# Kernel optimization log

Hardware: AMD Instinct MI355X
Metric: run time of the kernel (lower is better)

Reference implementation:

```python
import jax, jax.numpy as jnp
import numpy as np

DIM = 768
NUM_PROMPTS = 10
LATENT = 20
B = 16
N = 4096
EPS = 1e-5


def quick_gelu(x):
    return x * jax.nn.sigmoid(1.702 * x)


def layer_norm(x, g, b):
    mu = jnp.mean(x, axis=-1, keepdims=True)
    var = jnp.var(x, axis=-1, keepdims=True)
    return (x - mu) * jax.lax.rsqrt(var + EPS) * g + b


def setup_inputs() -> dict:
    key = jax.random.key(0)
    ks = jax.random.split(key, 12)
    s_in = 1.0 / np.sqrt(DIM)
    s_lat = 1.0 / np.sqrt(LATENT)
    s64 = 1.0 / np.sqrt(64)
    return {
        "x": jax.random.normal(ks[0], (B, NUM_PROMPTS + 1 + N, DIM), jnp.float32),
        "local_tokens": jax.random.normal(ks[1], (B, N, DIM), jnp.float32),
        # proj_down: Linear(dim, latent)
        "Wd": jax.random.uniform(ks[2], (DIM, LATENT), jnp.float32, -s_in, s_in),
        "bd": jnp.zeros((LATENT,), jnp.float32),
        # proj_up: Linear(latent, dim)
        "Wu": jax.random.uniform(ks[3], (LATENT, DIM), jnp.float32, -s_lat, s_lat),
        "bu": jnp.zeros((DIM,), jnp.float32),
        # global / local query projections: Linear(latent, latent)
        "Wgq": jax.random.uniform(ks[4], (LATENT, LATENT), jnp.float32, -s_lat, s_lat),
        "bgq": jnp.zeros((LATENT,), jnp.float32),
        "Wlq": jax.random.uniform(ks[5], (LATENT, LATENT), jnp.float32, -s_lat, s_lat),
        "blq": jnp.zeros((LATENT,), jnp.float32),
        # cls_analyzer: LN(latent) -> Linear(latent,64) -> GELU -> Linear(64,num_prompts) -> Sigmoid
        "ln_c_g": jnp.ones((LATENT,), jnp.float32),
        "ln_c_b": jnp.zeros((LATENT,), jnp.float32),
        "Wc1": jax.random.uniform(ks[6], (LATENT, 64), jnp.float32, -s_lat, s_lat),
        "bc1": jnp.zeros((64,), jnp.float32),
        "Wc2": jax.random.uniform(ks[7], (64, NUM_PROMPTS), jnp.float32, -s64, s64),
        "bc2": jnp.zeros((NUM_PROMPTS,), jnp.float32),
        # gl_balancer: LN(latent) -> Linear(latent,1) -> Sigmoid
        "ln_g_g": jnp.ones((LATENT,), jnp.float32),
        "ln_g_b": jnp.zeros((LATENT,), jnp.float32),
        "Wg": jax.random.uniform(ks[8], (LATENT, 1), jnp.float32, -s_lat, s_lat),
        "bg": jnp.zeros((1,), jnp.float32),
    }


def _attend(q, tokens, scale):
    # q: [B,P,d], tokens: [B,n,d]
    w = jax.nn.softmax(jnp.einsum('bpd,bnd->bpn', q, tokens) * scale, axis=-1)
    return jnp.einsum('bpn,bnd->bpd', w, tokens)


def reference(x, local_tokens, Wd, bd, Wu, bu, Wgq, bgq, Wlq, blq,
              ln_c_g, ln_c_b, Wc1, bc1, Wc2, bc2, ln_g_g, ln_g_b, Wg, bg):
    scale = LATENT ** (-0.5)
    x_latent = quick_gelu(x @ Wd + bd)            # [B, P+1+N, d]
    local_latent = quick_gelu(local_tokens @ Wd + bd)  # [B, N, d]

    prompts_latent = x_latent[:, :NUM_PROMPTS]              # [B,P,d]
    cls_latent = x_latent[:, NUM_PROMPTS:NUM_PROMPTS + 1]   # [B,1,d]
    global_img_latent = x_latent[:, NUM_PROMPTS + 1:]       # [B,N,d]

    cls_ln = layer_norm(cls_latent, ln_c_g, ln_c_b)
    prompt_importance = jax.nn.sigmoid(
        jax.nn.gelu(cls_ln @ Wc1 + bc1, approximate=False) @ Wc2 + bc2)  # [B,1,P]
    global_weight = jax.nn.sigmoid(layer_norm(cls_latent, ln_g_g, ln_g_b) @ Wg + bg)  # [B,1,1]

    global_context = _attend(prompts_latent @ Wgq + bgq, global_img_latent, scale)
    local_context = _attend(prompts_latent @ Wlq + blq, local_latent, scale)

    fused = global_weight * global_context + (1.0 - global_weight) * local_context
    enhanced = fused * jnp.swapaxes(prompt_importance, 1, 2)  # [B,P,d]

    combined = jnp.concatenate([enhanced, cls_latent, global_img_latent], axis=1)
    return combined @ Wu + bu
```

## Files before the change

### kernel.cpp

```cpp
#include <hip/hip_runtime.h>
#include <math.h>

#define DIM   768
#define LAT   20
#define NP    10
#define NB    16
#define SEQ   4096
#define SEQX  (NP + 1 + SEQ)
#define NXROWS (NB * SEQX)
#define NLROWS (NB * SEQ)
#define NROWS  (NXROWS + NLROWS)
#define EPSF  1e-5f

typedef __attribute__((ext_vector_type(8))) short  v8s;
typedef __attribute__((ext_vector_type(4))) float  v4f;
typedef __attribute__((ext_vector_type(4))) unsigned short u16x4;
typedef __attribute__((ext_vector_type(8))) unsigned short u16x8;

__device__ __forceinline__ float sigmoidf_(float z) { return 1.f / (1.f + __expf(-z)); }

__device__ __forceinline__ unsigned short bf16u(float v) {
    unsigned u = __builtin_bit_cast(unsigned, v);
    unsigned r = u + 0x7fffu + ((u >> 16) & 1u);
    return (unsigned short)(r >> 16);
}

__device__ __forceinline__ void gload_lds16(const void* g, void* s) {
    __builtin_amdgcn_global_load_lds(
        (const __attribute__((address_space(1))) unsigned int*)g,
        (__attribute__((address_space(3))) unsigned int*)s, 16, 0, 0);
}

__global__ __launch_bounds__(256) void k_wfrag(const float* __restrict__ Wd,
                                               unsigned short* __restrict__ wf)
{
    int slot = blockIdx.x * 256 + threadIdx.x;
    int fs = slot >> 7, rem = slot & 127;
    int nt = rem >> 6, l = rem & 63;
    int n = nt * 16 + (l & 15);
    int q = l >> 4;
    u16x8 w;
#pragma unroll
    for (int e = 0; e < 8; e++) {
        int k = fs * 32 + q * 8 + e;
        float v = (n < LAT) ? Wd[k * LAT + n] : 0.f;
        w[e] = bf16u(v);
    }
    *(u16x8*)&wf[slot * 8] = w;
}

#define WF_B    49152
#define SLOT_B  2048
#define RING_B  (4 * SLOT_B)

__global__ __launch_bounds__(256, 2) void k_down(const float* __restrict__ x,
                                                 const float* __restrict__ loc,
                                                 const unsigned short* __restrict__ wf,
                                                 const float* __restrict__ bd,
                                                 float* __restrict__ lat)
{
    __shared__ __align__(16) unsigned short lds[(WF_B + 4 * RING_B) / 2];
    const int tid = threadIdx.x, l = tid & 63, w = tid >> 6;

    {
        const char* g = (const char*)wf;
        char* s = (char*)lds;
#pragma unroll
        for (int i = 0; i < 12; ++i) {
            int off = i * 4096 + w * 1024;
            gload_lds16(g + off + l * 16, s + off);
        }
    }
    asm volatile("s_waitcnt vmcnt(0)" ::: "memory");
    __syncthreads();

    const int r0 = blockIdx.x * 64 + w * 16;
    if (r0 >= NROWS) return;
    const float* srcb = (r0 < NXROWS) ? x + (size_t)r0 * DIM
                                      : loc + (size_t)(r0 - NXROWS) * DIM;
    const float* gp = srcb + (size_t)(l & 15) * DIM + (l >> 4) * 8;
    char* ring = (char*)lds + WF_B + w * RING_B;

#pragma unroll
    for (int p = 0; p < 4; ++p) {
        gload_lds16(gp + p * 32,     ring + p * SLOT_B);
        gload_lds16(gp + p * 32 + 4, ring + p * SLOT_B + 1024);
    }

    v4f acc0 = {0.f, 0.f, 0.f, 0.f}, acc1 = {0.f, 0.f, 0.f, 0.f};

#define CVT8(A, F0, F1)                                                   \
    A[0] = (short)bf16u(F0.x); A[1] = (short)bf16u(F0.y);                 \
    A[2] = (short)bf16u(F0.z); A[3] = (short)bf16u(F0.w);                 \
    A[4] = (short)bf16u(F1.x); A[5] = (short)bf16u(F1.y);                 \
    A[6] = (short)bf16u(F1.z); A[7] = (short)bf16u(F1.w);

#define KSTEP(T, VMSTR) do {                                              \
    asm volatile("s_waitcnt " VMSTR ::: "memory");                        \
    float4 f0 = *(const float4*)(ring + ((T) & 3) * SLOT_B + l * 16);     \
    float4 f1 = *(const float4*)(ring + ((T) & 3) * SLOT_B + 1024 + l * 16); \
    v8s a; CVT8(a, f0, f1);                                               \
    v8s b0 = *(const v8s*)&lds[(((T) * 2 + 0) * 64 + l) * 8];             \
    v8s b1 = *(const v8s*)&lds[(((T) * 2 + 1) * 64 + l) * 8];             \
    acc0 = __builtin_amdgcn_mfma_f32_16x16x32_bf16(a, b0, acc0, 0, 0, 0); \
    acc1 = __builtin_amdgcn_mfma_f32_16x16x32_bf16(a, b1, acc1, 0, 0, 0); \
    if ((T) + 4 < 24) {                                                   \
        asm volatile("s_waitcnt lgkmcnt(0)" ::: "memory");                \
        gload_lds16(gp + ((T) + 4) * 32,     ring + ((T) & 3) * SLOT_B);  \
        gload_lds16(gp + ((T) + 4) * 32 + 4, ring + ((T) & 3) * SLOT_B + 1024); \
    }                                                                     \
} while (0)

    KSTEP(0,  "vmcnt(6)");  KSTEP(1,  "vmcnt(6)");  KSTEP(2,  "vmcnt(6)");
    KSTEP(3,  "vmcnt(6)");  KSTEP(4,  "vmcnt(6)");  KSTEP(5,  "vmcnt(6)");
    KSTEP(6,  "vmcnt(6)");  KSTEP(7,  "vmcnt(6)");  KSTEP(8,  "vmcnt(6)");
    KSTEP(9,  "vmcnt(6)");  KSTEP(10, "vmcnt(6)");  KSTEP(11, "vmcnt(6)");
    KSTEP(12, "vmcnt(6)");  KSTEP(13, "vmcnt(6)");  KSTEP(14, "vmcnt(6)");
    KSTEP(15, "vmcnt(6)");  KSTEP(16, "vmcnt(6)");  KSTEP(17, "vmcnt(6)");
    KSTEP(18, "vmcnt(6)");  KSTEP(19, "vmcnt(6)");  KSTEP(20, "vmcnt(6)");
    KSTEP(21, "vmcnt(4)");  KSTEP(22, "vmcnt(2)");  KSTEP(23, "vmcnt(0)");
#undef KSTEP
#undef CVT8

    int col = l & 15, half = l >> 4;
#pragma unroll
    for (int nt = 0; nt < 2; nt++) {
        int j = nt * 16 + col;
        if (j >= LAT) continue;
        float bdj = bd[j];
        v4f A = nt ? acc1 : acc0;
#pragma unroll
        for (int r = 0; r < 4; r++) {
            int rowg = r0 + half * 4 + r;
            float z = A[r] + bdj;
            lat[(size_t)rowg * LAT + j] = z * sigmoidf_(1.702f * z);
        }
    }
}

__global__ __launch_bounds__(192, 3) void k_up(const float* __restrict__ lat,
                                               const float* __restrict__ Wu,
                                               const float* __restrict__ bu,
                                               float* __restrict__ out)
{
    int t = threadIdx.x;
    float4 wu[LAT];
#pragma unroll
    for (int k = 0; k < LAT; k++) wu[k] = ((const float4*)Wu)[k * 192 + t];
    float4 bv = ((const float4*)bu)[t];

    __shared__ float latile[64 * LAT];
    int rowbase = blockIdx.x * 64;
    {
        const float4* src = (const float4*)(lat + (size_t)rowbase * LAT);
        for (int idx = t; idx < 320; idx += 192) ((float4*)latile)[idx] = src[idx];
    }
    __syncthreads();

    int idx0 = rowbase % SEQX;
    for (int i = 0; i < 64; i++) {
        int row = rowbase + i;
        if (row >= NXROWS) break;
        int idx = idx0 + i;
        if (idx >= SEQX) idx -= SEQX;
        if (idx < NP) continue;
        const float* lp = latile + i * LAT;
        float4 acc = bv;
#pragma unroll
        for (int k = 0; k < LAT; k++) {
            float v = lp[k];
            acc.x += v * wu[k].x; acc.y += v * wu[k].y;
            acc.z += v * wu[k].z; acc.w += v * wu[k].w;
        }
        ((float4*)out)[(size_t)row * 192 + t] = acc;
    }
}

__global__ __launch_bounds__(64) void k_small(const float* __restrict__ lat_x,
    const float* __restrict__ Wgq, const float* __restrict__ bgq,
    const float* __restrict__ Wlq, const float* __restrict__ blq,
    const float* __restrict__ lncg, const float* __restrict__ lncb,
    const float* __restrict__ Wc1, const float* __restrict__ bc1,
    const float* __restrict__ Wc2, const float* __restrict__ bc2,
    const float* __restrict__ lngg, const float* __restrict__ lngb,
    const float* __restrict__ Wg, const float* __restrict__ bg,
    float* __restrict__ qg, float* __restrict__ ql,
    float* __restrict__ imp, float* __restrict__ gw)
{
    int b = blockIdx.x, t = threadIdx.x;
    __shared__ float cls[LAT], clsln[LAT], h1[64];
    __shared__ float mu_s, rs_s;

    const float* cp = lat_x + (size_t)(b * SEQX + NP) * LAT;
    if (t < LAT) cls[t] = cp[t];
    __syncthreads();

    if (t == 0) {
        float m = 0.f;
        for (int k = 0; k < LAT; k++) m += cls[k];
        m /= LAT;
        float v = 0.f;
        for (int k = 0; k < LAT; k++) { float d = cls[k] - m; v += d * d; }
        v /= LAT;
        float rs = rsqrtf(v + EPSF);
        mu_s = m; rs_s = rs;
        float s = bg[0];
        for (int k = 0; k < LAT; k++)
            s += ((cls[k] - m) * rs * lngg[k] + lngb[k]) * Wg[k];
        gw[b] = sigmoidf_(s);
    }
    __syncthreads();
    if (t < LAT) clsln[t] = (cls[t] - mu_s) * rs_s * lncg[t] + lncb[t];
    __syncthreads();

    {
        float s = bc1[t];
        for (int k = 0; k < LAT; k++) s += clsln[k] * Wc1[k * 64 + t];
        h1[t] = 0.5f * s * (1.f + erff(s * 0.70710678118f));
    }
    __syncthreads();
    if (t < NP) {
        float s = bc2[t];
        for (int i = 0; i < 64; i++) s += h1[i] * Wc2[i * NP + t];
        imp[b * NP + t] = sigmoidf_(s);
    }
    for (int idx = t; idx < NP * LAT; idx += 64) {
        int p = idx / LAT, j = idx % LAT;
        const float* pl = lat_x + (size_t)(b * SEQX + p) * LAT;
        float sg = bgq[j], sl = blq[j];
        for (int k = 0; k < LAT; k++) {
            float v = pl[k];
            sg += v * Wgq[k * LAT + j];
            sl += v * Wlq[k * LAT + j];
        }
        qg[(b * NP + p) * LAT + j] = sg;
        ql[(b * NP + p) * LAT + j] = sl;
    }
}

__global__ __launch_bounds__(256) void k_attn(const float* __restrict__ lat_x,
                                              const float* __restrict__ lat_l,
                                              const float* __restrict__ qg,
                                              const float* __restrict__ ql,
                                              float* __restrict__ ctxg,
                                              float* __restrict__ ctxl)
{
    int b = blockIdx.x, p = blockIdx.y, ty = blockIdx.z;
    const float* tok = (ty == 0) ? lat_x + (size_t)(b * SEQX + NP + 1) * LAT
                                 : lat_l + (size_t)b * SEQ * LAT;
    const float* q = ((ty == 0) ? qg : ql) + (size_t)(b * NP + p) * LAT;
    float* ctx = ((ty == 0) ? ctxg : ctxl) + (size_t)(b * NP + p) * LAT;

    int t = threadIdx.x;
    __shared__ float qs[LAT];
    __shared__ float red[128];
    __shared__ float Ms;
    __shared__ float tot[21];
    if (t < LAT) qs[t] = q[t];
    __syncthreads();

    const float scale = 0.22360679775f;
    float lg[16];
    float lmax = -1e30f;
    for (int i = 0; i < 16; i++) {
        const float* tk = tok + (size_t)(t + 256 * i) * LAT;
        float s = 0.f;
#pragma unroll
        for (int k = 0; k < LAT; k++) s += qs[k] * tk[k];
        s *= scale;
        lg[i] = s;
        lmax = fmaxf(lmax, s);
    }
    int wave = t >> 6, lane = t & 63;
    for (int off = 32; off; off >>= 1) lmax = fmaxf(lmax, __shfl_down(lmax, off, 64));
    if (lane == 0) red[wave] = lmax;
    __syncthreads();
    if (t == 0) Ms = fmaxf(fmaxf(red[0], red[1]), fmaxf(red[2], red[3]));
    __syncthreads();
    float M = Ms;

    float vals[21];
#pragma unroll
    for (int j = 0; j < 21; j++) vals[j] = 0.f;
    for (int i = 0; i < 16; i++) {
        float w = __expf(lg[i] - M);
        vals[20] += w;
        const float* tk = tok + (size_t)(t + 256 * i) * LAT;
#pragma unroll
        for (int k = 0; k < LAT; k++) vals[k] += w * tk[k];
    }
#pragma unroll
    for (int j = 0; j < 21; j++) {
        float v = vals[j];
        for (int off = 32; off; off >>= 1) v += __shfl_down(v, off, 64);
        vals[j] = v;
    }
    __syncthreads();
    if (lane == 0)
        for (int j = 0; j < 21; j++) red[wave * 21 + j] = vals[j];
    __syncthreads();
    if (t < 21) tot[t] = red[t] + red[21 + t] + red[42 + t] + red[63 + t];
    __syncthreads();
    if (t < LAT) ctx[t] = tot[t] / tot[20];
}

__global__ __launch_bounds__(192) void k_prompt_out(const float* __restrict__ ctxg,
                                                    const float* __restrict__ ctxl,
                                                    const float* __restrict__ imp,
                                                    const float* __restrict__ gw,
                                                    const float* __restrict__ Wu,
                                                    const float* __restrict__ bu,
                                                    float* __restrict__ out)
{
    int b = blockIdx.x, p = blockIdx.y, t = threadIdx.x;
    __shared__ float enh[LAT];
    if (t < LAT) {
        float g = gw[b];
        size_t o = (size_t)(b * NP + p) * LAT + t;
        float e = g * ctxg[o] + (1.f - g) * ctxl[o];
        enh[t] = e * imp[b * NP + p];
    }
    __syncthreads();
    float4 acc = ((const float4*)bu)[t];
#pragma unroll
    for (int k = 0; k < LAT; k++) {
        float4 w = ((const float4*)Wu)[k * 192 + t];
        float e = enh[k];
        acc.x += e * w.x; acc.y += e * w.y; acc.z += e * w.z; acc.w += e * w.w;
    }
    ((float4*)out)[(size_t)(b * SEQX + p) * 192 + t] = acc;
}

extern "C" void kernel_launch(void* const* d_in, const int* in_sizes, int n_in,
                              void* d_out, int out_size, void* d_ws, size_t ws_size,
                              hipStream_t stream)
{
    const float* x    = (const float*)d_in[0];
    const float* loc  = (const float*)d_in[1];
    const float* Wd   = (const float*)d_in[2];
    const float* bd   = (const float*)d_in[3];
    const float* Wu   = (const float*)d_in[4];
    const float* bu   = (const float*)d_in[5];
    const float* Wgq  = (const float*)d_in[6];
    const float* bgq  = (const float*)d_in[7];
    const float* Wlq  = (const float*)d_in[8];
    const float* blq  = (const float*)d_in[9];
    const float* lncg = (const float*)d_in[10];
    const float* lncb = (const float*)d_in[11];
    const float* Wc1  = (const float*)d_in[12];
    const float* bc1  = (const float*)d_in[13];
    const float* Wc2  = (const float*)d_in[14];
    const float* bc2  = (const float*)d_in[15];
    const float* lngg = (const float*)d_in[16];
    const float* lngb = (const float*)d_in[17];
    const float* Wg   = (const float*)d_in[18];
    const float* bg   = (const float*)d_in[19];
    float* out = (float*)d_out;

    float* ws   = (float*)d_ws;
    float* lat_x = ws;
    float* lat_l = lat_x + (size_t)NXROWS * LAT;
    float* qg    = lat_l + (size_t)NLROWS * LAT;
    float* ql    = qg + NB * NP * LAT;
    float* ctxg  = ql + NB * NP * LAT;
    float* ctxl  = ctxg + NB * NP * LAT;
    float* impw  = ctxl + NB * NP * LAT;
    float* gww   = impw + NB * NP;
    unsigned short* wfrag = (unsigned short*)(gww + NB);

    k_wfrag<<<12, 256, 0, stream>>>(Wd, wfrag);
    k_down<<<(NROWS + 63) / 64, 256, 0, stream>>>(x, loc, wfrag, bd, lat_x);
    k_up<<<(NXROWS + 63) / 64, 192, 0, stream>>>(lat_x, Wu, bu, out);
    k_small<<<NB, 64, 0, stream>>>(lat_x, Wgq, bgq, Wlq, blq, lncg, lncb,
                                   Wc1, bc1, Wc2, bc2, lngg, lngb, Wg, bg,
                                   qg, ql, impw, gww);
    k_attn<<<dim3(NB, NP, 2), 256, 0, stream>>>(lat_x, lat_l, qg, ql, ctxg, ctxl);
    k_prompt_out<<<dim3(NB, NP), 192, 0, stream>>>(ctxg, ctxl, impw, gww, Wu, bu, out);
}
```

Measured before the change: 566.3 us.

## Restructure k_down staging into swizzled row-contiguous chunks with packed bf16 convert

The down-projection kernel now stages each 16-row block of input in 64-float chunks. Each lane loads contiguous 16-byte pieces of a row into an XOR-swizzled LDS layout with a two-slot double buffer, which replaces the previous scattered per-lane 16-byte loads. The float-to-bf16 conversion uses the hardware packed instruction v_cvt_pk_bf16_f32 instead of manual integer rounding. The up-projection kernel reads each latent row with five vector LDS loads instead of scalar reads. The aim is better global-load coalescing and fewer ALU instructions, at the cost of more complex addressing and a shallower prefetch depth in waits.

```diff
diff --git a/kernel.cpp b/kernel.cpp
--- a/kernel.cpp
+++ b/kernel.cpp
@@ -14,7 +14,7 @@
 
 typedef __attribute__((ext_vector_type(8))) short  v8s;
 typedef __attribute__((ext_vector_type(4))) float  v4f;
-typedef __attribute__((ext_vector_type(4))) unsigned short u16x4;
+typedef __attribute__((ext_vector_type(4))) unsigned int u32x4;
 typedef __attribute__((ext_vector_type(8))) unsigned short u16x8;
 
 __device__ __forceinline__ float sigmoidf_(float z) { return 1.f / (1.f + __expf(-z)); }
@@ -23,6 +23,12 @@
     unsigned u = __builtin_bit_cast(unsigned, v);
     unsigned r = u + 0x7fffu + ((u >> 16) & 1u);
     return (unsigned short)(r >> 16);
+}
+
+__device__ __forceinline__ unsigned cvtpk(float lo, float hi) {
+    unsigned r;
+    asm("v_cvt_pk_bf16_f32 %0, %1, %2" : "=v"(r) : "v"(lo), "v"(hi));
+    return r;
 }
 
 __device__ __forceinline__ void gload_lds16(const void* g, void* s) {
@@ -50,8 +56,7 @@
 }
 
 #define WF_B    49152
-#define SLOT_B  2048
-#define RING_B  (4 * SLOT_B)
+#define RING0   WF_B
 
 __global__ __launch_bounds__(256, 2) void k_down(const float* __restrict__ x,
                                                  const float* __restrict__ loc,
@@ -59,7 +64,7 @@
                                                  const float* __restrict__ bd,
                                                  float* __restrict__ lat)
 {
-    __shared__ __align__(16) unsigned short lds[(WF_B + 4 * RING_B) / 2];
+    __shared__ __align__(16) unsigned short lds[(WF_B + 4 * 8192) / 2];
     const int tid = threadIdx.x, l = tid & 63, w = tid >> 6;
 
     {
@@ -78,49 +83,70 @@
     if (r0 >= NROWS) return;
     const float* srcb = (r0 < NXROWS) ? x + (size_t)r0 * DIM
                                       : loc + (size_t)(r0 - NXROWS) * DIM;
-    const float* gp = srcb + (size_t)(l & 15) * DIM + (l >> 4) * 8;
-    char* ring = (char*)lds + WF_B + w * RING_B;
-
-#pragma unroll
-    for (int p = 0; p < 4; ++p) {
-        gload_lds16(gp + p * 32,     ring + p * SLOT_B);
-        gload_lds16(gp + p * 32 + 4, ring + p * SLOT_B + 1024);
-    }
+
+    const int rrq = l >> 4, cc = l & 15;
+    const float* Pp[4];
+#pragma unroll
+    for (int i = 0; i < 4; ++i) {
+        int rr = i * 4 + rrq;
+        Pp[i] = srcb + (size_t)rr * DIM + ((cc ^ (rr & 7)) * 4);
+    }
+
+    unsigned Aadr[2][2][2];
+    {
+        int rr = l & 15, q = l >> 4;
+#pragma unroll
+        for (int sl = 0; sl < 2; ++sl)
+#pragma unroll
+            for (int s = 0; s < 2; ++s)
+#pragma unroll
+                for (int h = 0; h < 2; ++h)
+                    Aadr[sl][s][h] = RING0 + w * 8192 + sl * 4096 + rr * 256
+                                   + (((s * 8 + 2 * q + h) ^ (rr & 7)) << 4);
+    }
+    const v8s* Bfr = (const v8s*)lds;
 
     v4f acc0 = {0.f, 0.f, 0.f, 0.f}, acc1 = {0.f, 0.f, 0.f, 0.f};
 
-#define CVT8(A, F0, F1)                                                   \
-    A[0] = (short)bf16u(F0.x); A[1] = (short)bf16u(F0.y);                 \
-    A[2] = (short)bf16u(F0.z); A[3] = (short)bf16u(F0.w);                 \
-    A[4] = (short)bf16u(F1.x); A[5] = (short)bf16u(F1.y);                 \
-    A[6] = (short)bf16u(F1.z); A[7] = (short)bf16u(F1.w);
-
-#define KSTEP(T, VMSTR) do {                                              \
-    asm volatile("s_waitcnt " VMSTR ::: "memory");                        \
-    float4 f0 = *(const float4*)(ring + ((T) & 3) * SLOT_B + l * 16);     \
-    float4 f1 = *(const float4*)(ring + ((T) & 3) * SLOT_B + 1024 + l * 16); \
-    v8s a; CVT8(a, f0, f1);                                               \
-    v8s b0 = *(const v8s*)&lds[(((T) * 2 + 0) * 64 + l) * 8];             \
-    v8s b1 = *(const v8s*)&lds[(((T) * 2 + 1) * 64 + l) * 8];             \
-    acc0 = __builtin_amdgcn_mfma_f32_16x16x32_bf16(a, b0, acc0, 0, 0, 0); \
-    acc1 = __builtin_amdgcn_mfma_f32_16x16x32_bf16(a, b1, acc1, 0, 0, 0); \
-    if ((T) + 4 < 24) {                                                   \
-        asm volatile("s_waitcnt lgkmcnt(0)" ::: "memory");                \
-        gload_lds16(gp + ((T) + 4) * 32,     ring + ((T) & 3) * SLOT_B);  \
-        gload_lds16(gp + ((T) + 4) * 32 + 4, ring + ((T) & 3) * SLOT_B + 1024); \
-    }                                                                     \
+#define STAGE(C, SL) do {                                                    \
+    asm volatile("s_waitcnt lgkmcnt(0)" ::: "memory");  \
+    char* sb_ = (char*)lds + RING0 + w * 8192 + (SL) * 4096;                 \
+    gload_lds16(Pp[0] + (C) * 64, sb_);                                      \
+    gload_lds16(Pp[1] + (C) * 64, sb_ + 1024);                               \
+    gload_lds16(Pp[2] + (C) * 64, sb_ + 2048);                               \
+    gload_lds16(Pp[3] + (C) * 64, sb_ + 3072);                               \
 } while (0)
 
-    KSTEP(0,  "vmcnt(6)");  KSTEP(1,  "vmcnt(6)");  KSTEP(2,  "vmcnt(6)");
-    KSTEP(3,  "vmcnt(6)");  KSTEP(4,  "vmcnt(6)");  KSTEP(5,  "vmcnt(6)");
-    KSTEP(6,  "vmcnt(6)");  KSTEP(7,  "vmcnt(6)");  KSTEP(8,  "vmcnt(6)");
-    KSTEP(9,  "vmcnt(6)");  KSTEP(10, "vmcnt(6)");  KSTEP(11, "vmcnt(6)");
-    KSTEP(12, "vmcnt(6)");  KSTEP(13, "vmcnt(6)");  KSTEP(14, "vmcnt(6)");
-    KSTEP(15, "vmcnt(6)");  KSTEP(16, "vmcnt(6)");  KSTEP(17, "vmcnt(6)");
-    KSTEP(18, "vmcnt(6)");  KSTEP(19, "vmcnt(6)");  KSTEP(20, "vmcnt(6)");
-    KSTEP(21, "vmcnt(4)");  KSTEP(22, "vmcnt(2)");  KSTEP(23, "vmcnt(0)");
+#define KSTEP(FS) do {                                                       \
+    float4 f0 = *(const float4*)((const char*)lds +                          \
+                                 Aadr[((FS) >> 1) & 1][(FS) & 1][0]);        \
+    float4 f1 = *(const float4*)((const char*)lds +                          \
+                                 Aadr[((FS) >> 1) & 1][(FS) & 1][1]);        \
+    u32x4 u_;                                                                \
+    u_[0] = cvtpk(f0.x, f0.y); u_[1] = cvtpk(f0.z, f0.w);                    \
+    u_[2] = cvtpk(f1.x, f1.y); u_[3] = cvtpk(f1.z, f1.w);                    \
+    v8s a_ = __builtin_bit_cast(v8s, u_);                                    \
+    v8s b0 = Bfr[((FS) * 2 + 0) * 64 + l];                                   \
+    v8s b1 = Bfr[((FS) * 2 + 1) * 64 + l];                                   \
+    acc0 = __builtin_amdgcn_mfma_f32_16x16x32_bf16(a_, b0, acc0, 0, 0, 0);   \
+    acc1 = __builtin_amdgcn_mfma_f32_16x16x32_bf16(a_, b1, acc1, 0, 0, 0);   \
+} while (0)
+
+#define CHUNK(C, WAITSTR) do {                                               \
+    asm volatile("s_waitcnt " WAITSTR ::: "memory");                         \
+    KSTEP(2 * (C)); KSTEP(2 * (C) + 1);                                      \
+    if ((C) < 10) STAGE((C) + 2, (C) & 1);                                   \
+} while (0)
+
+    STAGE(0, 0); STAGE(1, 1);
+
+    CHUNK(0,  "vmcnt(4)");  CHUNK(1,  "vmcnt(4)");  CHUNK(2,  "vmcnt(4)");
+    CHUNK(3,  "vmcnt(4)");  CHUNK(4,  "vmcnt(4)");  CHUNK(5,  "vmcnt(4)");
+    CHUNK(6,  "vmcnt(4)");  CHUNK(7,  "vmcnt(4)");  CHUNK(8,  "vmcnt(4)");
+    CHUNK(9,  "vmcnt(4)");  CHUNK(10, "vmcnt(4)");  CHUNK(11, "vmcnt(0)");
+#undef CHUNK
 #undef KSTEP
-#undef CVT8
+#undef STAGE
 
     int col = l & 15, half = l >> 4;
 #pragma unroll
@@ -149,7 +175,7 @@
     for (int k = 0; k < LAT; k++) wu[k] = ((const float4*)Wu)[k * 192 + t];
     float4 bv = ((const float4*)bu)[t];
 
-    __shared__ float latile[64 * LAT];
+    __shared__ __align__(16) float latile[64 * LAT];
     int rowbase = blockIdx.x * 64;
     {
         const float4* src = (const float4*)(lat + (size_t)rowbase * LAT);
@@ -164,11 +190,20 @@
         int idx = idx0 + i;
         if (idx >= SEQX) idx -= SEQX;
         if (idx < NP) continue;
-        const float* lp = latile + i * LAT;
+        const float4* lp4 = (const float4*)(latile + i * LAT);
+        float lv[LAT];
+        {
+            float4 t0 = lp4[0], t1 = lp4[1], t2 = lp4[2], t3 = lp4[3], t4 = lp4[4];
+            lv[0]=t0.x; lv[1]=t0.y; lv[2]=t0.z; lv[3]=t0.w;
+            lv[4]=t1.x; lv[5]=t1.y; lv[6]=t1.z; lv[7]=t1.w;
+            lv[8]=t2.x; lv[9]=t2.y; lv[10]=t2.z; lv[11]=t2.w;
+            lv[12]=t3.x; lv[13]=t3.y; lv[14]=t3.z; lv[15]=t3.w;
+            lv[16]=t4.x; lv[17]=t4.y; lv[18]=t4.z; lv[19]=t4.w;
+        }
         float4 acc = bv;
 #pragma unroll
         for (int k = 0; k < LAT; k++) {
-            float v = lp[k];
+            float v = lv[k];
             acc.x += v * wu[k].x; acc.y += v * wu[k].y;
             acc.z += v * wu[k].z; acc.w += v * wu[k].w;
         }
```

After: 558.5 us. About the same (-1.4%).
